# Kernel optimization log

Hardware: AMD Instinct MI355X
Metric: run time of the kernel (lower is better)

Reference implementation:

```python
import jax, jax.numpy as jnp
import numpy as np
import math

S = 8192
D = 128

def setup_inputs() -> dict:
    key = jax.random.key(0)
    kq, kk, kv = jax.random.split(key, 3)
    q = jax.random.normal(kq, (S, D), dtype=jnp.float32)
    k = jax.random.normal(kk, (S, D), dtype=jnp.float32)
    v = jax.random.normal(kv, (S, D), dtype=jnp.float32)
    return {"q": q, "k": k, "v": v}

def reference(q, k, v):
    # scores: [Sq, Sk], scaled by sqrt(head_dim)
    scale = 1.0 / math.sqrt(q.shape[1])
    scores = jnp.einsum('qd,kd->qk', q, k) * scale
    # causal mask: tril kept, strict upper triangle -> -inf (mask=True)
    causal = jnp.tril(jnp.ones((q.shape[0], k.shape[0]), dtype=bool))
    scores = jnp.where(causal, scores, -jnp.inf)
    # softmax over keys (dim=1), numerically stable
    attn = jax.nn.softmax(scores, axis=1)
    return jnp.einsum('qk,kd->qd', attn, v)
```

## Files before the change

### kernel.cpp

```cpp
#include <hip/hip_runtime.h>

#define S_TOTAL 8192
#define D_DIM   128
#define QBLK    256
#define NQT     32
#define NSPL    16
#define UNITS   512
#define TILEB   16384
#define QSCALE  0.12751879523178264f
#define NEG_BIG -1.0e30f
#define THR     8.0f

typedef __attribute__((ext_vector_type(8)))  short    bf16x8;
typedef __attribute__((ext_vector_type(16))) float    f32x16;
typedef __attribute__((ext_vector_type(4)))  float    f32x4;
typedef __attribute__((ext_vector_type(4)))  unsigned u32x4;

static __device__ __forceinline__ unsigned short f2bf(float f) {
    unsigned int u = __builtin_bit_cast(unsigned int, f);
    u += 0x7FFFu + ((u >> 16) & 1u);
    return (unsigned short)(u >> 16);
}
static __device__ __forceinline__ float bf2f(unsigned short u) {
    return __builtin_bit_cast(float, (unsigned int)u << 16);
}
static __device__ __forceinline__ void glds16(const void* g, void* l) {
    __builtin_amdgcn_global_load_lds(
        (const __attribute__((address_space(1))) void*)g,
        (__attribute__((address_space(3))) void*)l, 16, 0, 0);
}
static __device__ __forceinline__ unsigned pk2(float lo, float hi) {
    unsigned r;
    asm("v_cvt_pk_bf16_f32 %0, %1, %2" : "=v"(r) : "v"(lo), "v"(hi));
    return r;
}
static __device__ __forceinline__ void pl32swap(unsigned& x, unsigned& y) {
    asm("v_permlane32_swap_b32 %0, %1" : "+v"(x), "+v"(y));
}

__global__ __launch_bounds__(256)
void prep_all(const float* __restrict__ Q, const float* __restrict__ K,
              const float* __restrict__ V,
              unsigned short* __restrict__ Qbf,
              unsigned short* __restrict__ Kswz,
              unsigned short* __restrict__ Vt)
{
    __shared__ float sv[64 * 68];
    const int b   = (int)blockIdx.x;
    const int tid = threadIdx.x;

    if (b < 1024) {
        int i4 = b * 256 + tid;
        const float4 v = reinterpret_cast<const float4*>(Q)[i4];
        ushort4 o;
        o.x = f2bf(v.x * QSCALE); o.y = f2bf(v.y * QSCALE);
        o.z = f2bf(v.z * QSCALE); o.w = f2bf(v.w * QSCALE);
        reinterpret_cast<ushort4*>(Qbf)[i4] = o;
    } else if (b < 1536) {
        int c = (b - 1024) * 256 + tid;
        int t = c >> 10;
        int r = (c >> 4) & 63;
        int slot = c & 15;
        int d0 = (slot ^ (r & 15)) << 3;
        const float* src = K + ((size_t)t * 64 + r) * D_DIM + d0;
        float4 a  = *reinterpret_cast<const float4*>(src);
        float4 bq = *reinterpret_cast<const float4*>(src + 4);
        bf16x8 o;
        o[0] = (short)f2bf(a.x);  o[1] = (short)f2bf(a.y);
        o[2] = (short)f2bf(a.z);  o[3] = (short)f2bf(a.w);
        o[4] = (short)f2bf(bq.x); o[5] = (short)f2bf(bq.y);
        o[6] = (short)f2bf(bq.z); o[7] = (short)f2bf(bq.w);
        *reinterpret_cast<bf16x8*>(&Kswz[(size_t)c * 8]) = o;
    } else {
        int bb = b - 1536;
        int t = bb >> 1;
        int h = bb & 1;
        #pragma unroll
        for (int it = 0; it < 4; ++it) {
            int f4 = it * 256 + tid;
            int r   = f4 >> 4;
            int c16 = (f4 & 15) << 2;
            float4 v = *reinterpret_cast<const float4*>(
                V + ((size_t)t * 64 + r) * D_DIM + h * 64 + c16);
            sv[r * 68 + c16 + 0] = v.x;
            sv[r * 68 + c16 + 1] = v.y;
            sv[r * 68 + c16 + 2] = v.z;
            sv[r * 68 + c16 + 3] = v.w;
        }
        __syncthreads();
        #pragma unroll
        for (int ii = 0; ii < 2; ++ii) {
            int cl = tid * 2 + ii;
            int dl = cl >> 3;
            int slot = cl & 7;
            int d = h * 64 + dl;
            int k0 = (slot ^ (d & 7)) << 3;
            bf16x8 o;
            #pragma unroll
            for (int i = 0; i < 8; ++i) o[i] = (short)f2bf(sv[(k0 + i) * 68 + dl]);
            *reinterpret_cast<bf16x8*>(&Vt[(size_t)t * 8192 + ((size_t)(d * 8 + slot)) * 8]) = o;
        }
    }
}

#define PROC_SUB(QF, ACC, MR, LR, QSB)                                        \
  {                                                                           \
    const int qg_ = (QSB) + qc;                                               \
    f32x16 sc;                                                                \
    _Pragma("unroll")                                                         \
    for (int r = 0; r < 16; ++r) sc[r] = 0.0f;                                \
    {                                                                         \
      const int rK_ = kj * 32 + qc;                                           \
      __builtin_amdgcn_s_setprio(1);                                          \
      _Pragma("unroll")                                                       \
      for (int dc = 0; dc < 8; ++dc) {                                        \
        int slot_ = ((dc << 1) | hi) ^ (rK_ & 15);                            \
        bf16x8 kf_ = *reinterpret_cast<const bf16x8*>(                        \
            bK + (rK_ << 8) + (slot_ << 4));                                  \
        sc = __builtin_amdgcn_mfma_f32_32x32x16_bf16(kf_, QF[dc], sc, 0, 0, 0); \
      }                                                                       \
      __builtin_amdgcn_s_setprio(0);                                          \
    }                                                                         \
    if (kbase + 31 > (QSB)) {                                                 \
      _Pragma("unroll")                                                       \
      for (int r = 0; r < 16; ++r) {                                          \
        int kg_ = kbase + (r & 3) + 8 * (r >> 2) + 4 * hi;                    \
        if (kg_ > qg_) sc[r] = -INFINITY;                                     \
      }                                                                       \
    }                                                                         \
    float ma_ = fmaxf(fmaxf(sc[0],  sc[1]),  fmaxf(sc[2],  sc[3]));           \
    float mb_ = fmaxf(fmaxf(sc[4],  sc[5]),  fmaxf(sc[6],  sc[7]));           \
    float mc_ = fmaxf(fmaxf(sc[8],  sc[9]),  fmaxf(sc[10], sc[11]));          \
    float md_ = fmaxf(fmaxf(sc[12], sc[13]), fmaxf(sc[14], sc[15]));          \
    float mx_ = fmaxf(fmaxf(ma_, mb_), fmaxf(mc_, md_));                      \
    float tmax_ = fmaxf(mx_, __shfl_xor(mx_, 32));                            \
    if (__any(tmax_ > MR + THR)) {                                            \
      float mn_ = fmaxf(MR, tmax_);                                           \
      float fs_ = __builtin_amdgcn_exp2f(MR - mn_);                           \
      MR = mn_;                                                               \
      LR *= fs_;                                                              \
      _Pragma("unroll")                                                       \
      for (int dt = 0; dt < 4; ++dt)                                          \
        _Pragma("unroll")                                                     \
        for (int r = 0; r < 16; ++r) ACC[dt][r] *= fs_;                       \
    }                                                                         \
    float s0_ = 0.f, s1_ = 0.f, s2_ = 0.f, s3_ = 0.f;                         \
    _Pragma("unroll")                                                         \
    for (int r = 0; r < 16; r += 4) {                                         \
      float p0_ = __builtin_amdgcn_exp2f(sc[r + 0] - MR);                     \
      float p1_ = __builtin_amdgcn_exp2f(sc[r + 1] - MR);                     \
      float p2_ = __builtin_amdgcn_exp2f(sc[r + 2] - MR);                     \
      float p3_ = __builtin_amdgcn_exp2f(sc[r + 3] - MR);                     \
      sc[r + 0] = p0_; sc[r + 1] = p1_; sc[r + 2] = p2_; sc[r + 3] = p3_;     \
      s0_ += p0_; s1_ += p1_; s2_ += p2_; s3_ += p3_;                         \
    }                                                                         \
    float lt_ = (s0_ + s1_) + (s2_ + s3_);                                    \
    lt_ += __shfl_xor(lt_, 32);                                               \
    LR += lt_;                                                                \
    _Pragma("unroll")                                                         \
    for (int cl = 0; cl < 2; ++cl) {                                          \
      const int rb_ = cl * 8;                                                 \
      const int ck_ = kj * 2 + cl;                                            \
      unsigned pa_ = pk2(sc[rb_ + 0], sc[rb_ + 1]);                           \
      unsigned pb_ = pk2(sc[rb_ + 4], sc[rb_ + 5]);                           \
      unsigned pc_ = pk2(sc[rb_ + 2], sc[rb_ + 3]);                           \
      unsigned pd_ = pk2(sc[rb_ + 6], sc[rb_ + 7]);                           \
      pl32swap(pa_, pb_);                                                     \
      pl32swap(pc_, pd_);                                                     \
      u32x4 t4_ = {pa_, pc_, pb_, pd_};                                       \
      bf16x8 pf_ = __builtin_bit_cast(bf16x8, t4_);                           \
      __builtin_amdgcn_s_setprio(1);                                          \
      _Pragma("unroll")                                                       \
      for (int dt = 0; dt < 4; ++dt) {                                        \
        int dV_ = dt * 32 + qc;                                               \
        int slot_ = ((ck_ << 1) | hi) ^ (dV_ & 7);                            \
        bf16x8 vf_ = *reinterpret_cast<const bf16x8*>(                        \
            bV + (dV_ << 7) + (slot_ << 4));                                  \
        ACC[dt] = __builtin_amdgcn_mfma_f32_32x32x16_bf16(vf_, pf_, ACC[dt], 0, 0, 0); \
      }                                                                       \
      __builtin_amdgcn_s_setprio(0);                                          \
    }                                                                         \
  }

#define EPI_SUB(ACC, ROFF, MR, LR)                                            \
  {                                                                           \
    _Pragma("unroll")                                                         \
    for (int dt = 0; dt < 4; ++dt)                                            \
      _Pragma("unroll")                                                       \
      for (int i = 0; i < 8; ++i) {                                           \
        unsigned pk_ = pk2(ACC[dt][2 * i], ACC[dt][2 * i + 1]);               \
        int d_ = dt * 32 + (i & 1) * 2 + (i >> 1) * 8 + 4 * hi;               \
        *reinterpret_cast<unsigned*>(&sOw[qc * 136 + d_]) = pk_;              \
      }                                                                       \
    _Pragma("unroll")                                                         \
    for (int it = 0; it < 8; ++it) {                                          \
      int flat_ = it * 64 + lane;                                             \
      int q_  = flat_ >> 4;                                                   \
      int s8_ = flat_ & 15;                                                   \
      bf16x8 v_ = *reinterpret_cast<const bf16x8*>(&sOw[q_ * 136 + s8_ * 8]); \
      __builtin_nontemporal_store(v_, reinterpret_cast<bf16x8*>(              \
          OB + ((size_t)(w * 64 + (ROFF) + q_)) * D_DIM + s8_ * 8));          \
    }                                                                         \
    if (hi == 0) {                                                            \
      mpart[unit * QBLK + w * 64 + (ROFF) + qc] = MR;                         \
      lpart[unit * QBLK + w * 64 + (ROFF) + qc] = LR;                         \
    }                                                                         \
  }

__global__ __launch_bounds__(256, 2)
void attn16(const unsigned short* __restrict__ Qbf,
            const unsigned short* __restrict__ Kswz,
            const unsigned short* __restrict__ Vtswz,
            unsigned short* __restrict__ Opart,
            float* __restrict__ mpart, float* __restrict__ lpart)
{
    __shared__ char sbuf[2][2 * TILEB];

    const int bx = (int)blockIdx.x;
    const int p  = bx >> 4;
    const int s  = bx & 15;
    const int qt = (p < 16) ? (31 - p) : (p - 16);
    const int unit   = qt * NSPL + s;
    const int jtiles = 4 * qt + 4;

    const int tid  = threadIdx.x;
    const int w    = tid >> 6;
    const int lane = tid & 63;
    const int qc   = lane & 31;
    const int hi   = lane >> 5;

    const int qw0 = qt * QBLK + w * 64;

    bf16x8 qf0[8], qf1[8];
    #pragma unroll
    for (int dc = 0; dc < 8; ++dc) {
        qf0[dc] = *reinterpret_cast<const bf16x8*>(
            Qbf + (size_t)(qw0 + qc) * D_DIM + dc * 16 + hi * 8);
        qf1[dc] = *reinterpret_cast<const bf16x8*>(
            Qbf + (size_t)(qw0 + 32 + qc) * D_DIM + dc * 16 + hi * 8);
    }

    f32x16 acc0[4], acc1[4];
    #pragma unroll
    for (int dt = 0; dt < 4; ++dt)
        #pragma unroll
        for (int r = 0; r < 16; ++r) { acc0[dt][r] = 0.0f; acc1[dt][r] = 0.0f; }
    float m0r = NEG_BIG, l0r = 0.0f, m1r = NEG_BIG, l1r = 0.0f;

    auto STAGE = [&](int c, int j) {
        const char* gK = (const char*)Kswz + (size_t)j * TILEB;
        const char* gV = (const char*)Vtswz + (size_t)j * TILEB;
        char* lK = sbuf[c];
        char* lV = sbuf[c] + TILEB;
        #pragma unroll
        for (int it = 0; it < 4; ++it) {
            int goff = (it * 256 + tid) * 16;
            int loff = (it * 256 + (w << 6)) * 16;
            glds16(gK + goff, lK + loff);
            glds16(gV + goff, lV + loff);
        }
    };

    int j = s, c = 0;
    if (j < jtiles) {
        STAGE(0, j);
        __syncthreads();
        for (; j < jtiles; j += NSPL) {
            int jn = j + NSPL;
            if (jn < jtiles) STAGE(c ^ 1, jn);

            const char* bK = sbuf[c];
            const char* bV = sbuf[c] + TILEB;

            #pragma unroll
            for (int kj = 0; kj < 2; ++kj) {
                const int kbase = j * 64 + kj * 32;
                if (kbase <= qw0 + 63) {
                    if (kbase <= qw0 + 31)
                        PROC_SUB(qf0, acc0, m0r, l0r, qw0);
                    PROC_SUB(qf1, acc1, m1r, l1r, qw0 + 32);
                }
            }
            __syncthreads();
            c ^= 1;
        }
    }

    unsigned short* OB = Opart + (size_t)unit * (QBLK * D_DIM);
    unsigned short* sOw = reinterpret_cast<unsigned short*>(&sbuf[0][0])
                          + w * (32 * 136 + 16);
    EPI_SUB(acc0, 0,  m0r, l0r);
    EPI_SUB(acc1, 32, m1r, l1r);
}

__global__ __launch_bounds__(256)
void attn_mergeF(const unsigned short* __restrict__ Opart,
                 const float* __restrict__ mpart, const float* __restrict__ lpart,
                 float* __restrict__ Og)
{
    int tid = threadIdx.x;
    int row = blockIdx.x * 16 + (tid >> 4);
    int c8  = tid & 15;
    int qt    = row >> 8;
    int local = row & 255;
    int base  = qt * NSPL;

    float M = NEG_BIG;
    for (int s = 0; s < NSPL; ++s)
        M = fmaxf(M, mpart[(size_t)(base + s) * QBLK + local]);
    float L = 0.0f;
    for (int s = 0; s < NSPL; ++s)
        L += __builtin_amdgcn_exp2f(mpart[(size_t)(base + s) * QBLK + local] - M)
             * lpart[(size_t)(base + s) * QBLK + local];
    float invL = 1.0f / L;

    float a[8] = {0.f, 0.f, 0.f, 0.f, 0.f, 0.f, 0.f, 0.f};
    for (int s = 0; s < NSPL; ++s) {
        float e = __builtin_amdgcn_exp2f(mpart[(size_t)(base + s) * QBLK + local] - M);
        bf16x8 o = __builtin_nontemporal_load(reinterpret_cast<const bf16x8*>(
            &Opart[((size_t)(base + s) * QBLK + local) * D_DIM + c8 * 8]));
        #pragma unroll
        for (int i = 0; i < 8; ++i)
            a[i] += e * bf2f((unsigned short)o[i]);
    }
    float4 w0 = {a[0] * invL, a[1] * invL, a[2] * invL, a[3] * invL};
    float4 w1 = {a[4] * invL, a[5] * invL, a[6] * invL, a[7] * invL};
    float* dst = Og + (size_t)row * D_DIM + c8 * 8;
    *reinterpret_cast<float4*>(dst)     = w0;
    *reinterpret_cast<float4*>(dst + 4) = w1;
}

__global__ __launch_bounds__(256, 2)
void attn_f32(const float* __restrict__ Qg, const float* __restrict__ Kg,
              const float* __restrict__ Vg, float* __restrict__ Og)
{
    __shared__ unsigned short sK [64 * 128];
    __shared__ unsigned short sVt[128 * 64];
    __shared__ unsigned short sP [4 * 16 * 72];

    const int qt   = (int)gridDim.y - 1 - (int)blockIdx.y;
    const int tid  = threadIdx.x;
    const int w    = tid >> 6;
    const int lane = tid & 63;
    const int g    = lane >> 4;
    const int lr   = lane & 15;

    const int qrow_base  = qt * 64 + w * 16 + g * 4;
    const int q_frag_row = qt * 64 + w * 16 + lr;

    bf16x8 qa[4];
    #pragma unroll
    for (int dc = 0; dc < 4; ++dc) {
        const float* src = Qg + q_frag_row * D_DIM + dc * 32 + g * 8;
        bf16x8 v;
        #pragma unroll
        for (int i = 0; i < 8; ++i) v[i] = (short)f2bf(src[i]);
        qa[dc] = v;
    }

    f32x4 acc[8];
    #pragma unroll
    for (int dj = 0; dj < 8; ++dj) acc[dj] = f32x4{0.f, 0.f, 0.f, 0.f};
    float m_run[4], l_run[4];
    #pragma unroll
    for (int r = 0; r < 4; ++r) { m_run[r] = -INFINITY; l_run[r] = 0.0f; }

    const float scale = 0.08838834764831845f;
    const int jtiles = qt + 1;
    unsigned short* sPw = sP + w * (16 * 72);
    char* sKc = reinterpret_cast<char*>(sK);
    char* sVc = reinterpret_cast<char*>(sVt);

    for (int j = 0; j < jtiles; ++j) {
        __syncthreads();
        #pragma unroll
        for (int it = 0; it < 8; ++it) {
            int flat4 = it * 256 + tid;
            int r  = flat4 >> 5;
            int d0 = (flat4 & 31) << 2;
            const float4 kv = *reinterpret_cast<const float4*>(
                Kg + (j * 64 + r) * D_DIM + d0);
            ushort4 wv;
            wv.x = f2bf(kv.x); wv.y = f2bf(kv.y); wv.z = f2bf(kv.z); wv.w = f2bf(kv.w);
            int byte = (r << 8) | (((d0 >> 3) ^ (r & 15)) << 4) | ((d0 & 7) << 1);
            *reinterpret_cast<ushort4*>(sKc + byte) = wv;
        }
        {
            int d = tid & 127;
            int khalf = tid >> 7;
            #pragma unroll
            for (int it = 0; it < 8; ++it) {
                int k0 = it * 8 + khalf * 4;
                const float* vsrc = Vg + (j * 64 + k0) * D_DIM + d;
                ushort4 wv;
                wv.x = f2bf(vsrc[0 * D_DIM]); wv.y = f2bf(vsrc[1 * D_DIM]);
                wv.z = f2bf(vsrc[2 * D_DIM]); wv.w = f2bf(vsrc[3 * D_DIM]);
                int byte = (d << 7) | (((k0 >> 3) ^ (d & 7)) << 4) | ((k0 & 7) << 1);
                *reinterpret_cast<ushort4*>(sVc + byte) = wv;
            }
        }
        __syncthreads();

        f32x4 sf[4];
        #pragma unroll
        for (int kj = 0; kj < 4; ++kj) {
            f32x4 accs = f32x4{0.f, 0.f, 0.f, 0.f};
            #pragma unroll
            for (int dc = 0; dc < 4; ++dc) {
                int rowk = kj * 16 + lr;
                int slot = (dc * 4 + g) ^ lr;
                bf16x8 b = *reinterpret_cast<bf16x8*>(sKc + ((rowk << 8) | (slot << 4)));
                accs = __builtin_amdgcn_mfma_f32_16x16x32_bf16(qa[dc], b, accs, 0, 0, 0);
            }
            sf[kj] = accs;
        }
        #pragma unroll
        for (int kj = 0; kj < 4; ++kj)
            #pragma unroll
            for (int r = 0; r < 4; ++r)
                sf[kj][r] *= scale;
        if (j == qt) {
            #pragma unroll
            for (int kj = 0; kj < 4; ++kj) {
                int kglob = j * 64 + kj * 16 + lr;
                #pragma unroll
                for (int r = 0; r < 4; ++r)
                    if (kglob > qrow_base + r) sf[kj][r] = -INFINITY;
            }
        }
        float tmax[4];
        #pragma unroll
        for (int r = 0; r < 4; ++r)
            tmax[r] = fmaxf(fmaxf(sf[0][r], sf[1][r]), fmaxf(sf[2][r], sf[3][r]));
        #pragma unroll
        for (int off = 1; off < 16; off <<= 1)
            #pragma unroll
            for (int r = 0; r < 4; ++r)
                tmax[r] = fmaxf(tmax[r], __shfl_xor(tmax[r], off));
        float fsc[4], lt[4];
        #pragma unroll
        for (int r = 0; r < 4; ++r) {
            float mn = fmaxf(m_run[r], tmax[r]);
            fsc[r] = __expf(m_run[r] - mn);
            m_run[r] = mn;
            lt[r] = 0.0f;
        }
        #pragma unroll
        for (int kj = 0; kj < 4; ++kj)
            #pragma unroll
            for (int r = 0; r < 4; ++r) {
                float p = __expf(sf[kj][r] - m_run[r]);
                sf[kj][r] = p;
                lt[r] += p;
            }
        #pragma unroll
        for (int off = 1; off < 16; off <<= 1)
            #pragma unroll
            for (int r = 0; r < 4; ++r)
                lt[r] += __shfl_xor(lt[r], off);
        #pragma unroll
        for (int r = 0; r < 4; ++r)
            l_run[r] = l_run[r] * fsc[r] + lt[r];
        #pragma unroll
        for (int dj = 0; dj < 8; ++dj)
            #pragma unroll
            for (int r = 0; r < 4; ++r)
                acc[dj][r] *= fsc[r];
        #pragma unroll
        for (int kj = 0; kj < 4; ++kj)
            #pragma unroll
            for (int r = 0; r < 4; ++r)
                sPw[(g * 4 + r) * 72 + kj * 16 + lr] = f2bf(sf[kj][r]);
        bf16x8 pa[2];
        #pragma unroll
        for (int kc = 0; kc < 2; ++kc)
            pa[kc] = *reinterpret_cast<bf16x8*>(sPw + lr * 72 + kc * 32 + g * 8);
        #pragma unroll
        for (int dj = 0; dj < 8; ++dj) {
            #pragma unroll
            for (int kc = 0; kc < 2; ++kc) {
                int d = dj * 16 + lr;
                int slot = (kc * 4 + g) ^ (lr & 7);
                bf16x8 b = *reinterpret_cast<bf16x8*>(sVc + ((d << 7) | (slot << 4)));
                acc[dj] = __builtin_amdgcn_mfma_f32_16x16x32_bf16(pa[kc], b, acc[dj], 0, 0, 0);
            }
        }
    }
    #pragma unroll
    for (int r = 0; r < 4; ++r) {
        float inv = 1.0f / l_run[r];
        int row = qrow_base + r;
        #pragma unroll
        for (int dj = 0; dj < 8; ++dj)
            Og[row * D_DIM + dj * 16 + lr] = acc[dj][r] * inv;
    }
}

extern "C" void kernel_launch(void* const* d_in, const int* in_sizes, int n_in,
                              void* d_out, int out_size, void* d_ws, size_t ws_size,
                              hipStream_t stream)
{
    const float* Qg = (const float*)d_in[0];
    const float* Kg = (const float*)d_in[1];
    const float* Vg = (const float*)d_in[2];
    float* Og = (float*)d_out;

    const size_t bfElems = (size_t)S_TOTAL * D_DIM;
    const size_t need = 3 * bfElems * 2
                      + (size_t)UNITS * ((size_t)QBLK * D_DIM * 2
                                         + (size_t)QBLK * 8);

    if (d_ws == nullptr || ws_size < need) {
        hipLaunchKernelGGL(attn_f32, dim3(1, 128), dim3(256), 0, stream,
                           Qg, Kg, Vg, Og);
        return;
    }

    unsigned short* Qbf   = (unsigned short*)d_ws;
    unsigned short* Kswz  = Qbf + bfElems;
    unsigned short* Vt    = Kswz + bfElems;
    unsigned short* Opart = Vt + bfElems;
    float* mpart = (float*)(Opart + (size_t)UNITS * QBLK * D_DIM);
    float* lpart = mpart + (size_t)UNITS * QBLK;

    hipLaunchKernelGGL(prep_all, dim3(1792), dim3(256), 0, stream,
                       Qg, Kg, Vg, Qbf, Kswz, Vt);
    hipLaunchKernelGGL(attn16, dim3(UNITS), dim3(256), 0, stream,
                       Qbf, Kswz, Vt, Opart, mpart, lpart);
    hipLaunchKernelGGL(attn_mergeF, dim3(S_TOTAL / 16), dim3(256), 0, stream,
                       Opart, mpart, lpart, Og);
}
```

Baseline: 65.35 us.

## Fuse prep, attention and merge into one cooperative kernel with grid syncs

Replaces the three-kernel sequence (bf16 conversion/swizzle, split-K attention, merge) with a single cooperative launch of 512 blocks that separates the phases with grid.sync(). This removes two kernel launch boundaries and their drain and fill gaps. Partial outputs now use ordinary stores and loads instead of nontemporal ones, so they can stay in cache for the merge phase. The cost is grid-wide barrier overhead and the requirement that all 512 blocks be co-resident. If the cooperative launch fails, the code falls back to the three kernels.

```diff
diff --git a/kernel.cpp b/kernel.cpp
--- a/kernel.cpp
+++ b/kernel.cpp
@@ -1,4 +1,7 @@
 #include <hip/hip_runtime.h>
+#include <hip/hip_cooperative_groups.h>
+
+namespace cg = cooperative_groups;
 
 #define S_TOTAL 8192
 #define D_DIM   128
@@ -36,71 +39,6 @@
 }
 static __device__ __forceinline__ void pl32swap(unsigned& x, unsigned& y) {
     asm("v_permlane32_swap_b32 %0, %1" : "+v"(x), "+v"(y));
-}
-
-__global__ __launch_bounds__(256)
-void prep_all(const float* __restrict__ Q, const float* __restrict__ K,
-              const float* __restrict__ V,
-              unsigned short* __restrict__ Qbf,
-              unsigned short* __restrict__ Kswz,
-              unsigned short* __restrict__ Vt)
-{
-    __shared__ float sv[64 * 68];
-    const int b   = (int)blockIdx.x;
-    const int tid = threadIdx.x;
-
-    if (b < 1024) {
-        int i4 = b * 256 + tid;
-        const float4 v = reinterpret_cast<const float4*>(Q)[i4];
-        ushort4 o;
-        o.x = f2bf(v.x * QSCALE); o.y = f2bf(v.y * QSCALE);
-        o.z = f2bf(v.z * QSCALE); o.w = f2bf(v.w * QSCALE);
-        reinterpret_cast<ushort4*>(Qbf)[i4] = o;
-    } else if (b < 1536) {
-        int c = (b - 1024) * 256 + tid;
-        int t = c >> 10;
-        int r = (c >> 4) & 63;
-        int slot = c & 15;
-        int d0 = (slot ^ (r & 15)) << 3;
-        const float* src = K + ((size_t)t * 64 + r) * D_DIM + d0;
-        float4 a  = *reinterpret_cast<const float4*>(src);
-        float4 bq = *reinterpret_cast<const float4*>(src + 4);
-        bf16x8 o;
-        o[0] = (short)f2bf(a.x);  o[1] = (short)f2bf(a.y);
-        o[2] = (short)f2bf(a.z);  o[3] = (short)f2bf(a.w);
-        o[4] = (short)f2bf(bq.x); o[5] = (short)f2bf(bq.y);
-        o[6] = (short)f2bf(bq.z); o[7] = (short)f2bf(bq.w);
-        *reinterpret_cast<bf16x8*>(&Kswz[(size_t)c * 8]) = o;
-    } else {
-        int bb = b - 1536;
-        int t = bb >> 1;
-        int h = bb & 1;
-        #pragma unroll
-        for (int it = 0; it < 4; ++it) {
-            int f4 = it * 256 + tid;
-            int r   = f4 >> 4;
-            int c16 = (f4 & 15) << 2;
-            float4 v = *reinterpret_cast<const float4*>(
-                V + ((size_t)t * 64 + r) * D_DIM + h * 64 + c16);
-            sv[r * 68 + c16 + 0] = v.x;
-            sv[r * 68 + c16 + 1] = v.y;
-            sv[r * 68 + c16 + 2] = v.z;
-            sv[r * 68 + c16 + 3] = v.w;
-        }
-        __syncthreads();
-        #pragma unroll
-        for (int ii = 0; ii < 2; ++ii) {
-            int cl = tid * 2 + ii;
-            int dl = cl >> 3;
-            int slot = cl & 7;
-            int d = h * 64 + dl;
-            int k0 = (slot ^ (d & 7)) << 3;
-            bf16x8 o;
-            #pragma unroll
-            for (int i = 0; i < 8; ++i) o[i] = (short)f2bf(sv[(k0 + i) * 68 + dl]);
-            *reinterpret_cast<bf16x8*>(&Vt[(size_t)t * 8192 + ((size_t)(d * 8 + slot)) * 8]) = o;
-        }
-    }
 }
 
 #define PROC_SUB(QF, ACC, MR, LR, QSB)                                        \
@@ -198,14 +136,266 @@
       int q_  = flat_ >> 4;                                                   \
       int s8_ = flat_ & 15;                                                   \
       bf16x8 v_ = *reinterpret_cast<const bf16x8*>(&sOw[q_ * 136 + s8_ * 8]); \
-      __builtin_nontemporal_store(v_, reinterpret_cast<bf16x8*>(              \
-          OB + ((size_t)(w * 64 + (ROFF) + q_)) * D_DIM + s8_ * 8));          \
+      *reinterpret_cast<bf16x8*>(                                             \
+          OB + ((size_t)(w * 64 + (ROFF) + q_)) * D_DIM + s8_ * 8) = v_;      \
     }                                                                         \
     if (hi == 0) {                                                            \
       mpart[unit * QBLK + w * 64 + (ROFF) + qc] = MR;                         \
       lpart[unit * QBLK + w * 64 + (ROFF) + qc] = LR;                         \
     }                                                                         \
   }
+
+__global__ __launch_bounds__(256, 2)
+void attn_coop(const float* __restrict__ Qg, const float* __restrict__ Kg,
+               const float* __restrict__ Vg,
+               unsigned short* __restrict__ Qbf,
+               unsigned short* __restrict__ Kswz,
+               unsigned short* __restrict__ Vt,
+               unsigned short* __restrict__ Opart,
+               float* __restrict__ mpart, float* __restrict__ lpart,
+               float* __restrict__ Og)
+{
+    __shared__ char sbuf[2][2 * TILEB];
+    cg::grid_group grid = cg::this_grid();
+
+    const int bx  = (int)blockIdx.x;
+    const int tid = threadIdx.x;
+
+    {
+        #pragma unroll
+        for (int u = 0; u < 2; ++u) {
+            int i4 = (bx * 2 + u) * 256 + tid;
+            const float4 v = reinterpret_cast<const float4*>(Qg)[i4];
+            ushort4 o;
+            o.x = f2bf(v.x * QSCALE); o.y = f2bf(v.y * QSCALE);
+            o.z = f2bf(v.z * QSCALE); o.w = f2bf(v.w * QSCALE);
+            reinterpret_cast<ushort4*>(Qbf)[i4] = o;
+        }
+        {
+            int c = bx * 256 + tid;
+            int t = c >> 10;
+            int r = (c >> 4) & 63;
+            int slot = c & 15;
+            int d0 = (slot ^ (r & 15)) << 3;
+            const float* src = Kg + ((size_t)t * 64 + r) * D_DIM + d0;
+            float4 a  = *reinterpret_cast<const float4*>(src);
+            float4 bq = *reinterpret_cast<const float4*>(src + 4);
+            bf16x8 o;
+            o[0] = (short)f2bf(a.x);  o[1] = (short)f2bf(a.y);
+            o[2] = (short)f2bf(a.z);  o[3] = (short)f2bf(a.w);
+            o[4] = (short)f2bf(bq.x); o[5] = (short)f2bf(bq.y);
+            o[6] = (short)f2bf(bq.z); o[7] = (short)f2bf(bq.w);
+            *reinterpret_cast<bf16x8*>(&Kswz[(size_t)c * 8]) = o;
+        }
+        {
+            float* sv = reinterpret_cast<float*>(&sbuf[0][0]);
+            int t  = bx >> 2;
+            int h  = bx & 1;
+            int kh = (bx >> 1) & 1;
+            #pragma unroll
+            for (int u = 0; u < 2; ++u) {
+                int f4 = u * 256 + tid;
+                int r   = f4 >> 4;
+                int c16 = (f4 & 15) << 2;
+                float4 v = *reinterpret_cast<const float4*>(
+                    Vg + ((size_t)(t * 64 + kh * 32 + r)) * D_DIM + h * 64 + c16);
+                sv[r * 68 + c16 + 0] = v.x;
+                sv[r * 68 + c16 + 1] = v.y;
+                sv[r * 68 + c16 + 2] = v.z;
+                sv[r * 68 + c16 + 3] = v.w;
+            }
+            __syncthreads();
+            {
+                int dl = tid >> 2;
+                int sl = tid & 3;
+                int d  = h * 64 + dl;
+                int slot = ((kh << 2) | sl) ^ (d & 7);
+                bf16x8 o;
+                #pragma unroll
+                for (int i = 0; i < 8; ++i)
+                    o[i] = (short)f2bf(sv[(sl * 8 + i) * 68 + dl]);
+                *reinterpret_cast<bf16x8*>(
+                    &Vt[(size_t)t * 8192 + (size_t)(d * 8 + slot) * 8]) = o;
+            }
+            __syncthreads();
+        }
+    }
+    grid.sync();
+
+    {
+        const int p  = bx >> 4;
+        const int s  = bx & 15;
+        const int qt = (p < 16) ? (31 - p) : (p - 16);
+        const int unit   = qt * NSPL + s;
+        const int jtiles = 4 * qt + 4;
+
+        const int w    = tid >> 6;
+        const int lane = tid & 63;
+        const int qc   = lane & 31;
+        const int hi   = lane >> 5;
+
+        const int qw0 = qt * QBLK + w * 64;
+
+        bf16x8 qf0[8], qf1[8];
+        #pragma unroll
+        for (int dc = 0; dc < 8; ++dc) {
+            qf0[dc] = *reinterpret_cast<const bf16x8*>(
+                Qbf + (size_t)(qw0 + qc) * D_DIM + dc * 16 + hi * 8);
+            qf1[dc] = *reinterpret_cast<const bf16x8*>(
+                Qbf + (size_t)(qw0 + 32 + qc) * D_DIM + dc * 16 + hi * 8);
+        }
+
+        f32x16 acc0[4], acc1[4];
+        #pragma unroll
+        for (int dt = 0; dt < 4; ++dt)
+            #pragma unroll
+            for (int r = 0; r < 16; ++r) { acc0[dt][r] = 0.0f; acc1[dt][r] = 0.0f; }
+        float m0r = NEG_BIG, l0r = 0.0f, m1r = NEG_BIG, l1r = 0.0f;
+
+        auto STAGE = [&](int c, int j) {
+            const char* gK = (const char*)Kswz + (size_t)j * TILEB;
+            const char* gV = (const char*)Vt + (size_t)j * TILEB;
+            char* lK = sbuf[c];
+            char* lV = sbuf[c] + TILEB;
+            #pragma unroll
+            for (int it = 0; it < 4; ++it) {
+                int goff = (it * 256 + tid) * 16;
+                int loff = (it * 256 + (w << 6)) * 16;
+                glds16(gK + goff, lK + loff);
+                glds16(gV + goff, lV + loff);
+            }
+        };
+
+        int j = s, c = 0;
+        if (j < jtiles) {
+            STAGE(0, j);
+            __syncthreads();
+            for (; j < jtiles; j += NSPL) {
+                int jn = j + NSPL;
+                if (jn < jtiles) STAGE(c ^ 1, jn);
+
+                const char* bK = sbuf[c];
+                const char* bV = sbuf[c] + TILEB;
+
+                #pragma unroll
+                for (int kj = 0; kj < 2; ++kj) {
+                    const int kbase = j * 64 + kj * 32;
+                    if (kbase <= qw0 + 63) {
+                        if (kbase <= qw0 + 31)
+                            PROC_SUB(qf0, acc0, m0r, l0r, qw0);
+                        PROC_SUB(qf1, acc1, m1r, l1r, qw0 + 32);
+                    }
+                }
+                __syncthreads();
+                c ^= 1;
+            }
+        }
+
+        unsigned short* OB = Opart + (size_t)unit * (QBLK * D_DIM);
+        unsigned short* sOw = reinterpret_cast<unsigned short*>(&sbuf[0][0])
+                              + w * (32 * 136 + 16);
+        EPI_SUB(acc0, 0,  m0r, l0r);
+        EPI_SUB(acc1, 32, m1r, l1r);
+    }
+    grid.sync();
+
+    {
+        int row = bx * 16 + (tid >> 4);
+        int c8  = tid & 15;
+        int qt    = row >> 8;
+        int local = row & 255;
+        int base  = qt * NSPL;
+
+        float M = NEG_BIG;
+        for (int s = 0; s < NSPL; ++s)
+            M = fmaxf(M, mpart[(size_t)(base + s) * QBLK + local]);
+        float L = 0.0f;
+        for (int s = 0; s < NSPL; ++s)
+            L += __builtin_amdgcn_exp2f(mpart[(size_t)(base + s) * QBLK + local] - M)
+                 * lpart[(size_t)(base + s) * QBLK + local];
+        float invL = 1.0f / L;
+
+        float a[8] = {0.f, 0.f, 0.f, 0.f, 0.f, 0.f, 0.f, 0.f};
+        for (int s = 0; s < NSPL; ++s) {
+            float e = __builtin_amdgcn_exp2f(mpart[(size_t)(base + s) * QBLK + local] - M);
+            bf16x8 o = *reinterpret_cast<const bf16x8*>(
+                &Opart[((size_t)(base + s) * QBLK + local) * D_DIM + c8 * 8]);
+            #pragma unroll
+            for (int i = 0; i < 8; ++i)
+                a[i] += e * bf2f((unsigned short)o[i]);
+        }
+        float4 w0 = {a[0] * invL, a[1] * invL, a[2] * invL, a[3] * invL};
+        float4 w1 = {a[4] * invL, a[5] * invL, a[6] * invL, a[7] * invL};
+        float* dst = Og + (size_t)row * D_DIM + c8 * 8;
+        *reinterpret_cast<float4*>(dst)     = w0;
+        *reinterpret_cast<float4*>(dst + 4) = w1;
+    }
+}
+
+__global__ __launch_bounds__(256)
+void prep_all(const float* __restrict__ Q, const float* __restrict__ K,
+              const float* __restrict__ V,
+              unsigned short* __restrict__ Qbf,
+              unsigned short* __restrict__ Kswz,
+              unsigned short* __restrict__ Vt)
+{
+    __shared__ float sv[64 * 68];
+    const int b   = (int)blockIdx.x;
+    const int tid = threadIdx.x;
+
+    if (b < 1024) {
+        int i4 = b * 256 + tid;
+        const float4 v = reinterpret_cast<const float4*>(Q)[i4];
+        ushort4 o;
+        o.x = f2bf(v.x * QSCALE); o.y = f2bf(v.y * QSCALE);
+        o.z = f2bf(v.z * QSCALE); o.w = f2bf(v.w * QSCALE);
+        reinterpret_cast<ushort4*>(Qbf)[i4] = o;
+    } else if (b < 1536) {
+        int c = (b - 1024) * 256 + tid;
+        int t = c >> 10;
+        int r = (c >> 4) & 63;
+        int slot = c & 15;
+        int d0 = (slot ^ (r & 15)) << 3;
+        const float* src = K + ((size_t)t * 64 + r) * D_DIM + d0;
+        float4 a  = *reinterpret_cast<const float4*>(src);
+        float4 bq = *reinterpret_cast<const float4*>(src + 4);
+        bf16x8 o;
+        o[0] = (short)f2bf(a.x);  o[1] = (short)f2bf(a.y);
+        o[2] = (short)f2bf(a.z);  o[3] = (short)f2bf(a.w);
+        o[4] = (short)f2bf(bq.x); o[5] = (short)f2bf(bq.y);
+        o[6] = (short)f2bf(bq.z); o[7] = (short)f2bf(bq.w);
+        *reinterpret_cast<bf16x8*>(&Kswz[(size_t)c * 8]) = o;
+    } else {
+        int bb = b - 1536;
+        int t = bb >> 1;
+        int h = bb & 1;
+        #pragma unroll
+        for (int it = 0; it < 4; ++it) {
+            int f4 = it * 256 + tid;
+            int r   = f4 >> 4;
+            int c16 = (f4 & 15) << 2;
+            float4 v = *reinterpret_cast<const float4*>(
+                V + ((size_t)t * 64 + r) * D_DIM + h * 64 + c16);
+            sv[r * 68 + c16 + 0] = v.x;
+            sv[r * 68 + c16 + 1] = v.y;
+            sv[r * 68 + c16 + 2] = v.z;
+            sv[r * 68 + c16 + 3] = v.w;
+        }
+        __syncthreads();
+        #pragma unroll
+        for (int ii = 0; ii < 2; ++ii) {
+            int cl = tid * 2 + ii;
+            int dl = cl >> 3;
+            int slot = cl & 7;
+            int d = h * 64 + dl;
+            int k0 = (slot ^ (d & 7)) << 3;
+            bf16x8 o;
+            #pragma unroll
+            for (int i = 0; i < 8; ++i) o[i] = (short)f2bf(sv[(k0 + i) * 68 + dl]);
+            *reinterpret_cast<bf16x8*>(&Vt[(size_t)t * 8192 + ((size_t)(d * 8 + slot)) * 8]) = o;
+        }
+    }
+}
 
 __global__ __launch_bounds__(256, 2)
 void attn16(const unsigned short* __restrict__ Qbf,
@@ -317,8 +507,8 @@
     float a[8] = {0.f, 0.f, 0.f, 0.f, 0.f, 0.f, 0.f, 0.f};
     for (int s = 0; s < NSPL; ++s) {
         float e = __builtin_amdgcn_exp2f(mpart[(size_t)(base + s) * QBLK + local] - M);
-        bf16x8 o = __builtin_nontemporal_load(reinterpret_cast<const bf16x8*>(
-            &Opart[((size_t)(base + s) * QBLK + local) * D_DIM + c8 * 8]));
+        bf16x8 o = *reinterpret_cast<const bf16x8*>(
+            &Opart[((size_t)(base + s) * QBLK + local) * D_DIM + c8 * 8]);
         #pragma unroll
         for (int i = 0; i < 8; ++i)
             a[i] += e * bf2f((unsigned short)o[i]);
@@ -523,10 +713,19 @@
     float* mpart = (float*)(Opart + (size_t)UNITS * QBLK * D_DIM);
     float* lpart = mpart + (size_t)UNITS * QBLK;
 
-    hipLaunchKernelGGL(prep_all, dim3(1792), dim3(256), 0, stream,
-                       Qg, Kg, Vg, Qbf, Kswz, Vt);
-    hipLaunchKernelGGL(attn16, dim3(UNITS), dim3(256), 0, stream,
-                       Qbf, Kswz, Vt, Opart, mpart, lpart);
-    hipLaunchKernelGGL(attn_mergeF, dim3(S_TOTAL / 16), dim3(256), 0, stream,
-                       Opart, mpart, lpart, Og);
-}
+    void* args[10] = { (void*)&Qg, (void*)&Kg, (void*)&Vg,
+                       (void*)&Qbf, (void*)&Kswz, (void*)&Vt,
+                       (void*)&Opart, (void*)&mpart, (void*)&lpart,
+                       (void*)&Og };
+    hipError_t e = hipLaunchCooperativeKernel(
+        (const void*)attn_coop, dim3(UNITS), dim3(256), args, 0, stream);
+    if (e != hipSuccess) {
+        (void)hipGetLastError();
+        hipLaunchKernelGGL(prep_all, dim3(1792), dim3(256), 0, stream,
+                           Qg, Kg, Vg, Qbf, Kswz, Vt);
+        hipLaunchKernelGGL(attn16, dim3(UNITS), dim3(256), 0, stream,
+                           Qbf, Kswz, Vt, Opart, mpart, lpart);
+        hipLaunchKernelGGL(attn_mergeF, dim3(S_TOTAL / 16), dim3(256), 0, stream,
+                           Opart, mpart, lpart, Og);
+    }
+}
```

New measurement: 157.4 us. 141% more time.

## Fuse split-K merge into attention kernel via last-block atomic counter

Applied to the files above, without the earlier changes.

Removes the separate merge kernel launch: each attention block increments a per-query-tile counter after writing its partials, and the last of the 16 split blocks for that tile performs the log-sum-exp merge and writes the final fp32 output. The counter is zeroed in the prep kernel. This saves a launch and lets merging overlap with other tiles' compute, but puts the merge for a 256-row tile on a single block, which can lengthen the tail for the late-finishing tiles.

```diff
diff --git a/kernel.cpp b/kernel.cpp
--- a/kernel.cpp
+++ b/kernel.cpp
@@ -43,13 +43,15 @@
               const float* __restrict__ V,
               unsigned short* __restrict__ Qbf,
               unsigned short* __restrict__ Kswz,
-              unsigned short* __restrict__ Vt)
+              unsigned short* __restrict__ Vt,
+              int* __restrict__ cnt)
 {
     __shared__ float sv[64 * 68];
     const int b   = (int)blockIdx.x;
     const int tid = threadIdx.x;
 
     if (b < 1024) {
+        if (b == 0 && tid < NQT) cnt[tid] = 0;
         int i4 = b * 256 + tid;
         const float4 v = reinterpret_cast<const float4*>(Q)[i4];
         ushort4 o;
@@ -212,7 +214,8 @@
             const unsigned short* __restrict__ Kswz,
             const unsigned short* __restrict__ Vtswz,
             unsigned short* __restrict__ Opart,
-            float* __restrict__ mpart, float* __restrict__ lpart)
+            float* __restrict__ mpart, float* __restrict__ lpart,
+            int* __restrict__ cnt, float* __restrict__ Og)
 {
     __shared__ char sbuf[2][2 * TILEB];
 
@@ -291,43 +294,46 @@
                           + w * (32 * 136 + 16);
     EPI_SUB(acc0, 0,  m0r, l0r);
     EPI_SUB(acc1, 32, m1r, l1r);
-}
-
-__global__ __launch_bounds__(256)
-void attn_mergeF(const unsigned short* __restrict__ Opart,
-                 const float* __restrict__ mpart, const float* __restrict__ lpart,
-                 float* __restrict__ Og)
-{
-    int tid = threadIdx.x;
-    int row = blockIdx.x * 16 + (tid >> 4);
-    int c8  = tid & 15;
-    int qt    = row >> 8;
-    int local = row & 255;
-    int base  = qt * NSPL;
-
-    float M = NEG_BIG;
-    for (int s = 0; s < NSPL; ++s)
-        M = fmaxf(M, mpart[(size_t)(base + s) * QBLK + local]);
-    float L = 0.0f;
-    for (int s = 0; s < NSPL; ++s)
-        L += __builtin_amdgcn_exp2f(mpart[(size_t)(base + s) * QBLK + local] - M)
-             * lpart[(size_t)(base + s) * QBLK + local];
-    float invL = 1.0f / L;
-
-    float a[8] = {0.f, 0.f, 0.f, 0.f, 0.f, 0.f, 0.f, 0.f};
-    for (int s = 0; s < NSPL; ++s) {
-        float e = __builtin_amdgcn_exp2f(mpart[(size_t)(base + s) * QBLK + local] - M);
-        bf16x8 o = __builtin_nontemporal_load(reinterpret_cast<const bf16x8*>(
-            &Opart[((size_t)(base + s) * QBLK + local) * D_DIM + c8 * 8]));
-        #pragma unroll
-        for (int i = 0; i < 8; ++i)
-            a[i] += e * bf2f((unsigned short)o[i]);
-    }
-    float4 w0 = {a[0] * invL, a[1] * invL, a[2] * invL, a[3] * invL};
-    float4 w1 = {a[4] * invL, a[5] * invL, a[6] * invL, a[7] * invL};
-    float* dst = Og + (size_t)row * D_DIM + c8 * 8;
-    *reinterpret_cast<float4*>(dst)     = w0;
-    *reinterpret_cast<float4*>(dst + 4) = w1;
+
+    __threadfence();
+    __shared__ int sOld;
+    if (tid == 0) sOld = atomicAdd(&cnt[qt], 1);
+    __syncthreads();
+    if (sOld == NSPL - 1) {
+        __threadfence();
+        const int base = qt * NSPL;
+        const int c8   = tid & 15;
+        for (int g = 0; g < 16; ++g) {
+            int local = g * 16 + (tid >> 4);
+            float M = NEG_BIG;
+            #pragma unroll
+            for (int t = 0; t < NSPL; ++t)
+                M = fmaxf(M, mpart[(size_t)(base + t) * QBLK + local]);
+            float L = 0.0f;
+            #pragma unroll
+            for (int t = 0; t < NSPL; ++t)
+                L += __builtin_amdgcn_exp2f(mpart[(size_t)(base + t) * QBLK + local] - M)
+                     * lpart[(size_t)(base + t) * QBLK + local];
+            float invL = 1.0f / L;
+
+            float a[8] = {0.f, 0.f, 0.f, 0.f, 0.f, 0.f, 0.f, 0.f};
+            #pragma unroll
+            for (int t = 0; t < NSPL; ++t) {
+                float e = __builtin_amdgcn_exp2f(
+                    mpart[(size_t)(base + t) * QBLK + local] - M);
+                bf16x8 o = *reinterpret_cast<const bf16x8*>(
+                    &Opart[((size_t)(base + t) * QBLK + local) * D_DIM + c8 * 8]);
+                #pragma unroll
+                for (int i = 0; i < 8; ++i)
+                    a[i] += e * bf2f((unsigned short)o[i]);
+            }
+            float4 w0 = {a[0] * invL, a[1] * invL, a[2] * invL, a[3] * invL};
+            float4 w1 = {a[4] * invL, a[5] * invL, a[6] * invL, a[7] * invL};
+            float* dst = Og + ((size_t)(qt * QBLK + local)) * D_DIM + c8 * 8;
+            *reinterpret_cast<float4*>(dst)     = w0;
+            *reinterpret_cast<float4*>(dst + 4) = w1;
+        }
+    }
 }
 
 __global__ __launch_bounds__(256, 2)
@@ -508,7 +514,8 @@
     const size_t bfElems = (size_t)S_TOTAL * D_DIM;
     const size_t need = 3 * bfElems * 2
                       + (size_t)UNITS * ((size_t)QBLK * D_DIM * 2
-                                         + (size_t)QBLK * 8);
+                                         + (size_t)QBLK * 8)
+                      + NQT * sizeof(int);
 
     if (d_ws == nullptr || ws_size < need) {
         hipLaunchKernelGGL(attn_f32, dim3(1, 128), dim3(256), 0, stream,
@@ -522,11 +529,10 @@
     unsigned short* Opart = Vt + bfElems;
     float* mpart = (float*)(Opart + (size_t)UNITS * QBLK * D_DIM);
     float* lpart = mpart + (size_t)UNITS * QBLK;
+    int*   cnt   = (int*)(lpart + (size_t)UNITS * QBLK);
 
     hipLaunchKernelGGL(prep_all, dim3(1792), dim3(256), 0, stream,
-                       Qg, Kg, Vg, Qbf, Kswz, Vt);
+                       Qg, Kg, Vg, Qbf, Kswz, Vt, cnt);
     hipLaunchKernelGGL(attn16, dim3(UNITS), dim3(256), 0, stream,
-                       Qbf, Kswz, Vt, Opart, mpart, lpart);
-    hipLaunchKernelGGL(attn_mergeF, dim3(S_TOTAL / 16), dim3(256), 0, stream,
-                       Opart, mpart, lpart, Og);
-}
+                       Qbf, Kswz, Vt, Opart, mpart, lpart, cnt, Og);
+}
```

Result: slower. 173.2 us (+165.1%).
